# Performance work log

Hardware: AMD Instinct MI355X
Metric: run time of the kernel (lower is better)

## Reference

```python
import jax, jax.numpy as jnp
import numpy as np

BETA = 0.25
EPS = 1e-10


def setup_inputs() -> dict:
    key = jax.random.key(0)
    k1, k2 = jax.random.split(key)
    x = jax.random.normal(k1, (32, 64, 64, 64), dtype=jnp.float32)  # [B, C=embed_dim, H, W]
    embeddings = jax.random.normal(k2, (64, 512), dtype=jnp.float32)  # [embed_dim, K]
    return {"x": x, "embeddings": embeddings}


def reference(x, embeddings):
    B, C, H, W = x.shape
    K = embeddings.shape[1]
    sg = jax.lax.stop_gradient

    z_e = jnp.transpose(x, (0, 2, 3, 1))          # [B, H, W, C]
    z_flat = z_e.reshape(-1, C)                    # [N, C]

    # Squared L2 distances to codebook: ||z||^2 + ||e||^2 - 2 z.e
    dists = (
        jnp.sum(z_flat * z_flat, axis=1, keepdims=True)
        + jnp.sum(embeddings * embeddings, axis=0)
        - 2.0 * (z_flat @ embeddings)
    )                                              # [N, K]
    idx = jnp.argmin(dists, axis=1)                # [N]

    # Direct gather instead of one-hot matmul (same math)
    quantized = embeddings.T[idx].reshape(z_e.shape)  # [B, H, W, C]

    e_latent_loss = jnp.mean((sg(quantized) - z_e) ** 2)
    q_latent_loss = jnp.mean((quantized - sg(z_e)) ** 2)
    loss = q_latent_loss + BETA * e_latent_loss

    # Straight-through estimator
    quantized_st = z_e + sg(quantized - z_e)

    # Perplexity via codebook usage histogram (== mean of one-hot encodings)
    N = idx.shape[0]
    counts = jnp.zeros((K,), dtype=jnp.float32).at[idx].add(1.0)
    avg_probs = counts / N
    perplexity = jnp.exp(-jnp.sum(avg_probs * jnp.log(avg_probs + EPS)))

    quantized_out = jnp.transpose(quantized_st, (0, 3, 1, 2))  # [B, C, H, W]
    encoding_indices = idx.reshape(B, H, W)
    return loss, quantized_out, perplexity, encoding_indices
```

## Files before the change

### kernel.cpp

```cpp
#include <hip/hip_runtime.h>


#define B_ 32
#define C_ 64
#define HW_ 4096
#define K_ 512
#define N_ (B_ * HW_)
#define NC_ ((long long)N_ * C_)
#define ROWS_ 64
#define NBLK_ (N_ / ROWS_)
#define NSLOT_ 8

typedef __attribute__((ext_vector_type(8))) short short8;
typedef __attribute__((ext_vector_type(4))) float float4_t;


__device__ __forceinline__ unsigned short f2bf(float f) {
    unsigned u = __float_as_uint(f);
    u += 0x7fffu + ((u >> 16) & 1u);
    return (unsigned short)(u >> 16);
}
__device__ __forceinline__ float bf2f(unsigned short h) {
    return __uint_as_float(((unsigned)h) << 16);
}
__device__ __forceinline__ void merge2(float& m1, int& i1, float& m2,
                                       float om1, int oi1, float om2) {
    if (om1 < m1) { m2 = fminf(m1, om2); m1 = om1; i1 = oi1; }
    else          { m2 = fminf(m2, om1); }
}

__global__ __launch_bounds__(512) void vq_init(const float* __restrict__ emb,
                                               float* __restrict__ snmax_p,
                                               float* __restrict__ en,
                                               float* __restrict__ embT32,
                                               unsigned short* __restrict__ fBhi,
                                               unsigned short* __restrict__ fBlo,
                                               int* __restrict__ ghist8) {
    __shared__ float smax[8];
    int k = threadIdx.x;
    if (blockIdx.x < 64) {
        int c = blockIdx.x;
        float e = emb[c * K_ + k];
        embT32[k * C_ + c] = e;
        float s = -2.0f * e;
        unsigned short hi = f2bf(s);
        unsigned short lo = f2bf(s - bf2f(hi));
        int kk   = c >> 5;
        int lane = (((c & 31) >> 3) << 4) + (k & 15);
        int fb   = ((k >> 5) << 2) + (((k >> 4) & 1) << 1) + kk;
        int off  = (fb << 9) + (lane << 3) + (c & 7);
        fBhi[off] = hi;
        fBlo[off] = lo;
    } else {
#pragma unroll
        for (int s8 = 0; s8 < NSLOT_; ++s8) ghist8[(s8 << 9) + k] = 0;
        float s = 0.f;
#pragma unroll
        for (int c = 0; c < C_; ++c) {
            float e = emb[c * K_ + k];
            s += e * e;
        }
        en[k] = s;
        float m = s;
#pragma unroll
        for (int off = 32; off > 0; off >>= 1)
            m = fmaxf(m, __shfl_down(m, off, 64));
        if ((k & 63) == 0) smax[k >> 6] = m;
        __syncthreads();
        if (k == 0) {
            float mm = smax[0];
#pragma unroll
            for (int w2 = 1; w2 < 8; ++w2) mm = fmaxf(mm, smax[w2]);
            *snmax_p = 4.0f * mm;
        }
    }
}

#define STAGE(bufi, pp) do {                                                   \
    int eoff_ = ((pp) << 11) + (w << 9) + (lane << 3);                         \
    __builtin_amdgcn_global_load_lds(                                          \
        (const __attribute__((address_space(1))) unsigned*)(fBhi + eoff_),     \
        (__attribute__((address_space(3))) unsigned*)&LB[bufi][0][(w << 9)],   \
        16, 0, 0);                                                             \
    __builtin_amdgcn_global_load_lds(                                          \
        (const __attribute__((address_space(1))) unsigned*)(fBlo + eoff_),     \
        (__attribute__((address_space(3))) unsigned*)&LB[bufi][1][(w << 9)],   \
        16, 0, 0);                                                             \
} while (0)

#define COMP_LDS(bufi, pp) do {                                                \
    const unsigned short* hb_ = &LB[bufi][0][lane << 3];                       \
    const unsigned short* lb_ = &LB[bufi][1][lane << 3];                       \
    short8 h0_ = *(const short8*)(hb_);                                        \
    short8 h1_ = *(const short8*)(hb_ + 512);                                  \
    short8 g0_ = *(const short8*)(hb_ + 1024);                                 \
    short8 g1_ = *(const short8*)(hb_ + 1536);                                 \
    short8 l0_ = *(const short8*)(lb_);                                        \
    short8 l1_ = *(const short8*)(lb_ + 512);                                  \
    short8 q0_ = *(const short8*)(lb_ + 1024);                                 \
    short8 q1_ = *(const short8*)(lb_ + 1536);                                 \
    const int cb_ = ((pp) << 5) + ln15;                                        \
    float env0_ = sEn[cb_];                                                    \
    float env1_ = sEn[cb_ + 16];                                               \
    float4_t a0 = {env0_, env0_, env0_, env0_};                                \
    float4_t a1 = {0.f, 0.f, 0.f, 0.f};                                        \
    float4_t b0 = {env1_, env1_, env1_, env1_};                                \
    float4_t b1 = {0.f, 0.f, 0.f, 0.f};                                        \
    a0 = __builtin_amdgcn_mfma_f32_16x16x32_bf16(al0, h0_, a0, 0, 0, 0);       \
    a1 = __builtin_amdgcn_mfma_f32_16x16x32_bf16(al1, h1_, a1, 0, 0, 0);       \
    b0 = __builtin_amdgcn_mfma_f32_16x16x32_bf16(al0, g0_, b0, 0, 0, 0);       \
    b1 = __builtin_amdgcn_mfma_f32_16x16x32_bf16(al1, g1_, b1, 0, 0, 0);       \
    a0 = __builtin_amdgcn_mfma_f32_16x16x32_bf16(ah0, l0_, a0, 0, 0, 0);       \
    a1 = __builtin_amdgcn_mfma_f32_16x16x32_bf16(ah1, l1_, a1, 0, 0, 0);       \
    b0 = __builtin_amdgcn_mfma_f32_16x16x32_bf16(ah0, q0_, b0, 0, 0, 0);       \
    b1 = __builtin_amdgcn_mfma_f32_16x16x32_bf16(ah1, q1_, b1, 0, 0, 0);       \
    a0 = __builtin_amdgcn_mfma_f32_16x16x32_bf16(ah0, h0_, a0, 0, 0, 0);       \
    a1 = __builtin_amdgcn_mfma_f32_16x16x32_bf16(ah1, h1_, a1, 0, 0, 0);       \
    b0 = __builtin_amdgcn_mfma_f32_16x16x32_bf16(ah0, g0_, b0, 0, 0, 0);       \
    b1 = __builtin_amdgcn_mfma_f32_16x16x32_bf16(ah1, g1_, b1, 0, 0, 0);       \
    _Pragma("unroll")                                                          \
    for (int reg = 0; reg < 4; ++reg) {                                        \
        float vv = a0[reg] + a1[reg];                                          \
        bool  lt = vv < m1[reg];                                               \
        float mx = fmaxf(vv, m1[reg]);                                         \
        m2[reg] = fminf(m2[reg], mx);                                          \
        m1[reg] = fminf(m1[reg], vv);                                          \
        i1[reg] = lt ? cb_ : i1[reg];                                          \
    }                                                                          \
    _Pragma("unroll")                                                          \
    for (int reg = 0; reg < 4; ++reg) {                                        \
        float vv = b0[reg] + b1[reg];                                          \
        bool  lt = vv < m1[reg];                                               \
        float mx = fmaxf(vv, m1[reg]);                                         \
        m2[reg] = fminf(m2[reg], mx);                                          \
        m1[reg] = fminf(m1[reg], vv);                                          \
        i1[reg] = lt ? (cb_ + 16) : i1[reg];                                   \
    }                                                                          \
} while (0)

__global__ __launch_bounds__(256) void vq_argmin(const float* __restrict__ x,
                                                 const float* __restrict__ en_g,
                                                 const float* __restrict__ embT32,
                                                 const unsigned short* __restrict__ fBhi,
                                                 const unsigned short* __restrict__ fBlo,
                                                 const float* __restrict__ snmax_p,
                                                 float* __restrict__ out_q,
                                                 float* __restrict__ out_idx,
                                                 int* __restrict__ ghist8,
                                                 double* __restrict__ ssepart) {
    __shared__ unsigned short LB[2][2][2048];
    __shared__ float sEn[K_];
    __shared__ float znrow[ROWS_];
    __shared__ int   biarr[ROWS_];
    __shared__ int   flaglist[ROWS_];
    __shared__ float wsse[4];
    __shared__ int   nflag;

    const int t    = threadIdx.x;
    const int lane = t & 63;
    const int w    = t >> 6;
    const int ln15 = lane & 15;
    const int quad = lane >> 4;
    const int n0   = blockIdx.x * ROWS_;
    const int b    = n0 >> 12;
    const int hw0  = n0 & 4095;
    const float* xbase = x + ((size_t)b << 18) + hw0;
    const int myrow = (w << 4) + ln15;

    if (t == 0) nflag = 0;
    sEn[t]       = en_g[t];
    sEn[256 + t] = en_g[256 + t];

    STAGE(0, 0);
    STAGE(1, 1);

    float v0[8], v1[8];
#pragma unroll
    for (int j = 0; j < 8; ++j) {
        v0[j] = xbase[((size_t)((quad << 3) + j) << 12) + myrow];
        v1[j] = xbase[((size_t)(32 + (quad << 3) + j) << 12) + myrow];
    }
    short8 ah0, al0, ah1, al1;
    float znacc = 0.f;
#pragma unroll
    for (int j = 0; j < 8; ++j) {
        unsigned short h0 = f2bf(v0[j]);
        ah0[j] = (short)h0;
        al0[j] = (short)f2bf(v0[j] - bf2f(h0));
        unsigned short h1 = f2bf(v1[j]);
        ah1[j] = (short)h1;
        al1[j] = (short)f2bf(v1[j] - bf2f(h1));
        znacc += v0[j] * v0[j] + v1[j] * v1[j];
    }
    znacc += __shfl_xor(znacc, 16, 64);
    znacc += __shfl_xor(znacc, 32, 64);
    if (quad == 0) znrow[myrow] = znacc;
    __syncthreads();

    const float snm = *snmax_p;

    float m1[4], m2[4];
    int   i1[4];
#pragma unroll
    for (int reg = 0; reg < 4; ++reg) {
        m1[reg] = 3.4e38f; m2[reg] = 3.4e38f; i1[reg] = 0;
    }

#pragma unroll 2
    for (int p = 0; p < 16; ++p) {
        const int bufi = p & 1;
        COMP_LDS(bufi, p);
        __syncthreads();
        if (p < 14) STAGE(bufi, p + 2);
    }

#pragma unroll
    for (int reg = 0; reg < 4; ++reg) {
        float a1v = m1[reg], a2v = m2[reg];
        int   ai  = i1[reg];
#pragma unroll
        for (int s = 1; s < 16; s <<= 1) {
            float o1 = __shfl_xor(a1v, s, 16);
            int   oi = __shfl_xor(ai, s, 16);
            float o2 = __shfl_xor(a2v, s, 16);
            merge2(a1v, ai, a2v, o1, oi, o2);
        }
        if (ln15 == 0) {
            int row = (w << 4) + (quad << 2) + reg;
            float znr = znrow[row];
            float W = 1.4e-4f * __builtin_sqrtf(znr * snm) + 1e-3f;
            biarr[row] = ai;
            if (a2v > a1v + W) {
                out_idx[n0 + row] = (float)ai;
            } else {
                int pos = atomicAdd(&nflag, 1);
                flaglist[pos] = row;
            }
        }
    }
    __syncthreads();

    int nf = nflag;
    for (int f = w; f < nf; f += 4) {
        int r = flaglist[f];
        float zl = xbase[((size_t)lane << 12) + r];
        float d[8];
#pragma unroll
        for (int j = 0; j < 8; ++j) d[j] = 0.f;
        for (int c4 = 0; c4 < 16; ++c4) {
            float z0 = __shfl(zl, (c4 << 2) + 0, 64);
            float z1 = __shfl(zl, (c4 << 2) + 1, 64);
            float z2 = __shfl(zl, (c4 << 2) + 2, 64);
            float z3 = __shfl(zl, (c4 << 2) + 3, 64);
#pragma unroll
            for (int j = 0; j < 8; ++j) {
                float4_t e = *(const float4_t*)(embT32 + ((((lane << 3) + j) << 6) + (c4 << 2)));
                d[j] = fmaf(z0, e[0], d[j]);
                d[j] = fmaf(z1, e[1], d[j]);
                d[j] = fmaf(z2, e[2], d[j]);
                d[j] = fmaf(z3, e[3], d[j]);
            }
        }
        float znr = znrow[r];
        float best = 3.4e38f;
        int   bidx = 0;
#pragma unroll
        for (int j = 0; j < 8; ++j) {
            int k = (lane << 3) + j;
            float dist = (znr + sEn[k]) - 2.f * d[j];
            if (dist < best) { best = dist; bidx = k; }
        }
#pragma unroll
        for (int off = 32; off > 0; off >>= 1) {
            float ov = __shfl_down(best, off, 64);
            int   oi = __shfl_down(bidx, off, 64);
            if (ov < best || (ov == best && oi < bidx)) { best = ov; bidx = oi; }
        }
        if (lane == 0) {
            biarr[r] = bidx;
            out_idx[n0 + r] = (float)bidx;
        }
    }
    __syncthreads();

    const int code  = biarr[myrow];
    const float* eb = embT32 + (code << 6) + (quad << 3);
    float4_t e0 = *(const float4_t*)(eb);
    float4_t e1 = *(const float4_t*)(eb + 4);
    float4_t e2 = *(const float4_t*)(eb + 32);
    float4_t e3 = *(const float4_t*)(eb + 36);
    float* qrow = out_q + ((size_t)b << 18) + hw0 + myrow;
    float sacc = 0.f;
#pragma unroll
    for (int j = 0; j < 4; ++j) {
        int c0 = (quad << 3) + j;
        int c1 = (quad << 3) + 4 + j;
        float zA = bf2f((unsigned short)ah0[j])     + bf2f((unsigned short)al0[j]);
        float zB = bf2f((unsigned short)ah0[4 + j]) + bf2f((unsigned short)al0[4 + j]);
        float dA = e0[j] - zA, dB = e1[j] - zB;
        sacc += dA * dA + dB * dB;
        qrow[(size_t)c0 << 12] = e0[j];
        qrow[(size_t)c1 << 12] = e1[j];
        float zC = bf2f((unsigned short)ah1[j])     + bf2f((unsigned short)al1[j]);
        float zD = bf2f((unsigned short)ah1[4 + j]) + bf2f((unsigned short)al1[4 + j]);
        float dC = e2[j] - zC, dD = e3[j] - zD;
        sacc += dC * dC + dD * dD;
        qrow[(size_t)(32 + c0) << 12] = e2[j];
        qrow[(size_t)(32 + c1) << 12] = e3[j];
    }
#pragma unroll
    for (int off = 32; off > 0; off >>= 1)
        sacc += __shfl_down(sacc, off, 64);
    if (lane == 0) wsse[w] = sacc;
    __syncthreads();

    if (t == 0)
        ssepart[blockIdx.x] = (double)wsse[0] + (double)wsse[1]
                            + (double)wsse[2] + (double)wsse[3];
    if (t < ROWS_)
        __hip_atomic_fetch_add(&ghist8[((blockIdx.x & (NSLOT_ - 1)) << 9) + biarr[t]],
                               1, __ATOMIC_RELAXED, __HIP_MEMORY_SCOPE_AGENT);
}

__global__ __launch_bounds__(512) void vq_final(const int* __restrict__ ghist8,
                                                const double* __restrict__ ssepart,
                                                float* __restrict__ out_loss,
                                                float* __restrict__ out_perp) {
    __shared__ float  wsf[8];
    __shared__ double wsd[8];
    int t = threadIdx.x;
    int hsum = 0;
#pragma unroll
    for (int s8 = 0; s8 < NSLOT_; ++s8)
        hsum += ghist8[(s8 << 9) + t];
    float p = (float)hsum / (float)N_;
    float s = p * logf(p + 1e-10f);
    double d = ssepart[t] + ssepart[t + 512] + ssepart[t + 1024] + ssepart[t + 1536];
#pragma unroll
    for (int off = 32; off > 0; off >>= 1) {
        s += __shfl_down(s, off, 64);
        d += __shfl_down(d, off, 64);
    }
    if ((t & 63) == 0) { wsf[t >> 6] = s; wsd[t >> 6] = d; }
    __syncthreads();
    if (t == 0) {
        float  S = 0.f;
        double D = 0.0;
#pragma unroll
        for (int w = 0; w < 8; ++w) { S += wsf[w]; D += wsd[w]; }
        *out_perp = expf(-S);
        *out_loss = (float)(1.25 * D / (double)NC_);
    }
}

extern "C" void kernel_launch(void* const* d_in, const int* in_sizes, int n_in,
                              void* d_out, int out_size, void* d_ws, size_t ws_size,
                              hipStream_t stream) {
    const float* x   = (const float*)d_in[0];
    const float* emb = (const float*)d_in[1];

    float* out      = (float*)d_out;
    float* out_loss = out;
    float* out_q    = out + 1;
    float* out_perp = out + 1 + (size_t)N_ * C_;
    float* out_idx  = out + 2 + (size_t)N_ * C_;

    char* ws = (char*)d_ws;
    float*          snmax_p  = (float*)(ws + 56);
    float*          en       = (float*)(ws + 2112);
    float*          embT32   = (float*)(ws + 4160);
    unsigned short* fBhi     = (unsigned short*)(ws + 135232);
    unsigned short* fBlo     = (unsigned short*)(ws + 200768);
    int*            ghist8   = (int*)(ws + 266304);
    double*         ssepart  = (double*)(ws + 282688);

    vq_init<<<65, 512, 0, stream>>>(emb, snmax_p, en, embT32, fBhi, fBlo, ghist8);
    vq_argmin<<<NBLK_, 256, 0, stream>>>(x, en, embT32, fBhi, fBlo, snmax_p,
                                         out_q, out_idx, ghist8, ssepart);
    vq_final<<<1, 512, 0, stream>>>(ghist8, ssepart, out_loss, out_perp);
}
```

Baseline: 155.0 us.

## Register-block two row tiles per wave to reuse codebook LDS fragments

Each wave now processes two 16-row tiles instead of one, so every block covers 128 rows and there are half as many blocks. The bf16 hi/lo codebook fragments read from LDS once per step feed MFMAs for both row tiles. This halves LDS reads and codebook staging per row. In exchange, registers for x fragments and running argmin state double, which may lower occupancy. The final reduction is adjusted for the smaller number of per-block partial sums.

Measured after the change: 190.5 us. +22.9%, slower.

```diff
diff --git a/kernel.cpp b/kernel.cpp
--- a/kernel.cpp
+++ b/kernel.cpp
@@ -7,7 +7,7 @@
 #define K_ 512
 #define N_ (B_ * HW_)
 #define NC_ ((long long)N_ * C_)
-#define ROWS_ 64
+#define ROWS_ 128
 #define NBLK_ (N_ / ROWS_)
 #define NSLOT_ 8
 
@@ -102,39 +102,42 @@
     const int cb_ = ((pp) << 5) + ln15;                                        \
     float env0_ = sEn[cb_];                                                    \
     float env1_ = sEn[cb_ + 16];                                               \
-    float4_t a0 = {env0_, env0_, env0_, env0_};                                \
-    float4_t a1 = {0.f, 0.f, 0.f, 0.f};                                        \
-    float4_t b0 = {env1_, env1_, env1_, env1_};                                \
-    float4_t b1 = {0.f, 0.f, 0.f, 0.f};                                        \
-    a0 = __builtin_amdgcn_mfma_f32_16x16x32_bf16(al0, h0_, a0, 0, 0, 0);       \
-    a1 = __builtin_amdgcn_mfma_f32_16x16x32_bf16(al1, h1_, a1, 0, 0, 0);       \
-    b0 = __builtin_amdgcn_mfma_f32_16x16x32_bf16(al0, g0_, b0, 0, 0, 0);       \
-    b1 = __builtin_amdgcn_mfma_f32_16x16x32_bf16(al1, g1_, b1, 0, 0, 0);       \
-    a0 = __builtin_amdgcn_mfma_f32_16x16x32_bf16(ah0, l0_, a0, 0, 0, 0);       \
-    a1 = __builtin_amdgcn_mfma_f32_16x16x32_bf16(ah1, l1_, a1, 0, 0, 0);       \
-    b0 = __builtin_amdgcn_mfma_f32_16x16x32_bf16(ah0, q0_, b0, 0, 0, 0);       \
-    b1 = __builtin_amdgcn_mfma_f32_16x16x32_bf16(ah1, q1_, b1, 0, 0, 0);       \
-    a0 = __builtin_amdgcn_mfma_f32_16x16x32_bf16(ah0, h0_, a0, 0, 0, 0);       \
-    a1 = __builtin_amdgcn_mfma_f32_16x16x32_bf16(ah1, h1_, a1, 0, 0, 0);       \
-    b0 = __builtin_amdgcn_mfma_f32_16x16x32_bf16(ah0, g0_, b0, 0, 0, 0);       \
-    b1 = __builtin_amdgcn_mfma_f32_16x16x32_bf16(ah1, g1_, b1, 0, 0, 0);       \
     _Pragma("unroll")                                                          \
-    for (int reg = 0; reg < 4; ++reg) {                                        \
-        float vv = a0[reg] + a1[reg];                                          \
-        bool  lt = vv < m1[reg];                                               \
-        float mx = fmaxf(vv, m1[reg]);                                         \
-        m2[reg] = fminf(m2[reg], mx);                                          \
-        m1[reg] = fminf(m1[reg], vv);                                          \
-        i1[reg] = lt ? cb_ : i1[reg];                                          \
-    }                                                                          \
-    _Pragma("unroll")                                                          \
-    for (int reg = 0; reg < 4; ++reg) {                                        \
-        float vv = b0[reg] + b1[reg];                                          \
-        bool  lt = vv < m1[reg];                                               \
-        float mx = fmaxf(vv, m1[reg]);                                         \
-        m2[reg] = fminf(m2[reg], mx);                                          \
-        m1[reg] = fminf(m1[reg], vv);                                          \
-        i1[reg] = lt ? (cb_ + 16) : i1[reg];                                   \
+    for (int rt = 0; rt < 2; ++rt) {                                           \
+        float4_t a0 = {env0_, env0_, env0_, env0_};                            \
+        float4_t a1 = {0.f, 0.f, 0.f, 0.f};                                    \
+        float4_t b0 = {env1_, env1_, env1_, env1_};                            \
+        float4_t b1 = {0.f, 0.f, 0.f, 0.f};                                    \
+        a0 = __builtin_amdgcn_mfma_f32_16x16x32_bf16(al0[rt], h0_, a0, 0,0,0); \
+        a1 = __builtin_amdgcn_mfma_f32_16x16x32_bf16(al1[rt], h1_, a1, 0,0,0); \
+        b0 = __builtin_amdgcn_mfma_f32_16x16x32_bf16(al0[rt], g0_, b0, 0,0,0); \
+        b1 = __builtin_amdgcn_mfma_f32_16x16x32_bf16(al1[rt], g1_, b1, 0,0,0); \
+        a0 = __builtin_amdgcn_mfma_f32_16x16x32_bf16(ah0[rt], l0_, a0, 0,0,0); \
+        a1 = __builtin_amdgcn_mfma_f32_16x16x32_bf16(ah1[rt], l1_, a1, 0,0,0); \
+        b0 = __builtin_amdgcn_mfma_f32_16x16x32_bf16(ah0[rt], q0_, b0, 0,0,0); \
+        b1 = __builtin_amdgcn_mfma_f32_16x16x32_bf16(ah1[rt], q1_, b1, 0,0,0); \
+        a0 = __builtin_amdgcn_mfma_f32_16x16x32_bf16(ah0[rt], h0_, a0, 0,0,0); \
+        a1 = __builtin_amdgcn_mfma_f32_16x16x32_bf16(ah1[rt], h1_, a1, 0,0,0); \
+        b0 = __builtin_amdgcn_mfma_f32_16x16x32_bf16(ah0[rt], g0_, b0, 0,0,0); \
+        b1 = __builtin_amdgcn_mfma_f32_16x16x32_bf16(ah1[rt], g1_, b1, 0,0,0); \
+        _Pragma("unroll")                                                      \
+        for (int reg = 0; reg < 4; ++reg) {                                    \
+            float vv = a0[reg] + a1[reg];                                      \
+            bool  lt = vv < m1[rt][reg];                                       \
+            float mx = fmaxf(vv, m1[rt][reg]);                                 \
+            m2[rt][reg] = fminf(m2[rt][reg], mx);                              \
+            m1[rt][reg] = fminf(m1[rt][reg], vv);                              \
+            i1[rt][reg] = lt ? cb_ : i1[rt][reg];                              \
+        }                                                                      \
+        _Pragma("unroll")                                                      \
+        for (int reg = 0; reg < 4; ++reg) {                                    \
+            float vv = b0[reg] + b1[reg];                                      \
+            bool  lt = vv < m1[rt][reg];                                       \
+            float mx = fmaxf(vv, m1[rt][reg]);                                 \
+            m2[rt][reg] = fminf(m2[rt][reg], mx);                              \
+            m1[rt][reg] = fminf(m1[rt][reg], vv);                              \
+            i1[rt][reg] = lt ? (cb_ + 16) : i1[rt][reg];                       \
+        }                                                                      \
     }                                                                          \
 } while (0)
 
@@ -165,7 +168,6 @@
     const int b    = n0 >> 12;
     const int hw0  = n0 & 4095;
     const float* xbase = x + ((size_t)b << 18) + hw0;
-    const int myrow = (w << 4) + ln15;
 
     if (t == 0) nflag = 0;
     sEn[t]       = en_g[t];
@@ -174,37 +176,43 @@
     STAGE(0, 0);
     STAGE(1, 1);
 
-    float v0[8], v1[8];
-#pragma unroll
-    for (int j = 0; j < 8; ++j) {
-        v0[j] = xbase[((size_t)((quad << 3) + j) << 12) + myrow];
-        v1[j] = xbase[((size_t)(32 + (quad << 3) + j) << 12) + myrow];
-    }
-    short8 ah0, al0, ah1, al1;
-    float znacc = 0.f;
-#pragma unroll
-    for (int j = 0; j < 8; ++j) {
-        unsigned short h0 = f2bf(v0[j]);
-        ah0[j] = (short)h0;
-        al0[j] = (short)f2bf(v0[j] - bf2f(h0));
-        unsigned short h1 = f2bf(v1[j]);
-        ah1[j] = (short)h1;
-        al1[j] = (short)f2bf(v1[j] - bf2f(h1));
-        znacc += v0[j] * v0[j] + v1[j] * v1[j];
-    }
-    znacc += __shfl_xor(znacc, 16, 64);
-    znacc += __shfl_xor(znacc, 32, 64);
-    if (quad == 0) znrow[myrow] = znacc;
+    short8 ah0[2], al0[2], ah1[2], al1[2];
+#pragma unroll
+    for (int rt = 0; rt < 2; ++rt) {
+        const int mr = (w << 5) + (rt << 4) + ln15;
+        float v0[8], v1[8];
+#pragma unroll
+        for (int j = 0; j < 8; ++j) {
+            v0[j] = xbase[((size_t)((quad << 3) + j) << 12) + mr];
+            v1[j] = xbase[((size_t)(32 + (quad << 3) + j) << 12) + mr];
+        }
+        float znacc = 0.f;
+#pragma unroll
+        for (int j = 0; j < 8; ++j) {
+            unsigned short h0 = f2bf(v0[j]);
+            ah0[rt][j] = (short)h0;
+            al0[rt][j] = (short)f2bf(v0[j] - bf2f(h0));
+            unsigned short h1 = f2bf(v1[j]);
+            ah1[rt][j] = (short)h1;
+            al1[rt][j] = (short)f2bf(v1[j] - bf2f(h1));
+            znacc += v0[j] * v0[j] + v1[j] * v1[j];
+        }
+        znacc += __shfl_xor(znacc, 16, 64);
+        znacc += __shfl_xor(znacc, 32, 64);
+        if (quad == 0) znrow[mr] = znacc;
+    }
     __syncthreads();
 
     const float snm = *snmax_p;
 
-    float m1[4], m2[4];
-    int   i1[4];
-#pragma unroll
-    for (int reg = 0; reg < 4; ++reg) {
-        m1[reg] = 3.4e38f; m2[reg] = 3.4e38f; i1[reg] = 0;
-    }
+    float m1[2][4], m2[2][4];
+    int   i1[2][4];
+#pragma unroll
+    for (int rt = 0; rt < 2; ++rt)
+#pragma unroll
+        for (int reg = 0; reg < 4; ++reg) {
+            m1[rt][reg] = 3.4e38f; m2[rt][reg] = 3.4e38f; i1[rt][reg] = 0;
+        }
 
 #pragma unroll 2
     for (int p = 0; p < 16; ++p) {
@@ -215,9 +223,11 @@
     }
 
 #pragma unroll
+    for (int rt = 0; rt < 2; ++rt)
+#pragma unroll
     for (int reg = 0; reg < 4; ++reg) {
-        float a1v = m1[reg], a2v = m2[reg];
-        int   ai  = i1[reg];
+        float a1v = m1[rt][reg], a2v = m2[rt][reg];
+        int   ai  = i1[rt][reg];
 #pragma unroll
         for (int s = 1; s < 16; s <<= 1) {
             float o1 = __shfl_xor(a1v, s, 16);
@@ -226,7 +236,7 @@
             merge2(a1v, ai, a2v, o1, oi, o2);
         }
         if (ln15 == 0) {
-            int row = (w << 4) + (quad << 2) + reg;
+            int row = (w << 5) + (rt << 4) + (quad << 2) + reg;
             float znr = znrow[row];
             float W = 1.4e-4f * __builtin_sqrtf(znr * snm) + 1e-3f;
             biarr[row] = ai;
@@ -283,30 +293,34 @@
     }
     __syncthreads();
 
-    const int code  = biarr[myrow];
-    const float* eb = embT32 + (code << 6) + (quad << 3);
-    float4_t e0 = *(const float4_t*)(eb);
-    float4_t e1 = *(const float4_t*)(eb + 4);
-    float4_t e2 = *(const float4_t*)(eb + 32);
-    float4_t e3 = *(const float4_t*)(eb + 36);
-    float* qrow = out_q + ((size_t)b << 18) + hw0 + myrow;
     float sacc = 0.f;
 #pragma unroll
-    for (int j = 0; j < 4; ++j) {
-        int c0 = (quad << 3) + j;
-        int c1 = (quad << 3) + 4 + j;
-        float zA = bf2f((unsigned short)ah0[j])     + bf2f((unsigned short)al0[j]);
-        float zB = bf2f((unsigned short)ah0[4 + j]) + bf2f((unsigned short)al0[4 + j]);
-        float dA = e0[j] - zA, dB = e1[j] - zB;
-        sacc += dA * dA + dB * dB;
-        qrow[(size_t)c0 << 12] = e0[j];
-        qrow[(size_t)c1 << 12] = e1[j];
-        float zC = bf2f((unsigned short)ah1[j])     + bf2f((unsigned short)al1[j]);
-        float zD = bf2f((unsigned short)ah1[4 + j]) + bf2f((unsigned short)al1[4 + j]);
-        float dC = e2[j] - zC, dD = e3[j] - zD;
-        sacc += dC * dC + dD * dD;
-        qrow[(size_t)(32 + c0) << 12] = e2[j];
-        qrow[(size_t)(32 + c1) << 12] = e3[j];
+    for (int rt = 0; rt < 2; ++rt) {
+        const int mr   = (w << 5) + (rt << 4) + ln15;
+        const int code = biarr[mr];
+        const float* eb = embT32 + (code << 6) + (quad << 3);
+        float4_t e0 = *(const float4_t*)(eb);
+        float4_t e1 = *(const float4_t*)(eb + 4);
+        float4_t e2 = *(const float4_t*)(eb + 32);
+        float4_t e3 = *(const float4_t*)(eb + 36);
+        float* qrow = out_q + ((size_t)b << 18) + hw0 + mr;
+#pragma unroll
+        for (int j = 0; j < 4; ++j) {
+            int c0 = (quad << 3) + j;
+            int c1 = (quad << 3) + 4 + j;
+            float zA = bf2f((unsigned short)ah0[rt][j])     + bf2f((unsigned short)al0[rt][j]);
+            float zB = bf2f((unsigned short)ah0[rt][4 + j]) + bf2f((unsigned short)al0[rt][4 + j]);
+            float dA = e0[j] - zA, dB = e1[j] - zB;
+            sacc += dA * dA + dB * dB;
+            qrow[(size_t)c0 << 12] = e0[j];
+            qrow[(size_t)c1 << 12] = e1[j];
+            float zC = bf2f((unsigned short)ah1[rt][j])     + bf2f((unsigned short)al1[rt][j]);
+            float zD = bf2f((unsigned short)ah1[rt][4 + j]) + bf2f((unsigned short)al1[rt][4 + j]);
+            float dC = e2[j] - zC, dD = e3[j] - zD;
+            sacc += dC * dC + dD * dD;
+            qrow[(size_t)(32 + c0) << 12] = e2[j];
+            qrow[(size_t)(32 + c1) << 12] = e3[j];
+        }
     }
 #pragma unroll
     for (int off = 32; off > 0; off >>= 1)
@@ -335,7 +349,7 @@
         hsum += ghist8[(s8 << 9) + t];
     float p = (float)hsum / (float)N_;
     float s = p * logf(p + 1e-10f);
-    double d = ssepart[t] + ssepart[t + 512] + ssepart[t + 1024] + ssepart[t + 1536];
+    double d = ssepart[t] + ssepart[t + 512];
 #pragma unroll
     for (int off = 32; off > 0; off >>= 1) {
         s += __shfl_down(s, off, 64);
```
